# Optimization experiments

Measured on AMD Instinct MI355X. Metric: run time of the kernel, lower is better.

Reference implementation:

```python
import jax, jax.numpy as jnp
import numpy as np

H = 1024; NH = 16; L = 4; K = 128; N = 65536
ADIM_MOVE = 9; ADIM_TURN = 4; S = 2 * K + 2


def setup_inputs() -> dict:
    key = jax.random.key(0)
    ks = jax.random.split(key, 24)
    s = 0.02
    d = {}
    d['x'] = jax.random.normal(ks[0], (1, H), jnp.float32)
    d['memory_vectors'] = jax.random.normal(ks[1], (N, H), jnp.float32)
    d['memory_next_vectors'] = jax.random.normal(ks[2], (N, H), jnp.float32)
    d['memory_surprises'] = jax.random.uniform(ks[3], (N,), jnp.float32)
    d['memory_rewards'] = jax.random.normal(ks[4], (N,), jnp.float32)
    d['rand_noise'] = jax.random.uniform(ks[5], (N,), jnp.float32)
    d['action_idx_move'] = jax.random.randint(ks[6], (N,), 0, ADIM_MOVE)
    d['action_idx_turn'] = jax.random.randint(ks[7], (N,), 0, ADIM_TURN)
    d['start_token'] = jax.random.uniform(ks[8], (1, H)) * 2 - 1
    d['pos_emb'] = jax.random.uniform(ks[9], (S, H)) * 2 - 1
    d['in_proj_w'] = jax.random.normal(ks[10], (L, 3 * H, H)) * s
    d['in_proj_b'] = jnp.zeros((L, 3 * H))
    d['out_w'] = jax.random.normal(ks[11], (L, H, H)) * s
    d['out_b'] = jnp.zeros((L, H))
    d['ln1_w'] = jnp.ones((L, H)); d['ln1_b'] = jnp.zeros((L, H))
    d['ln2_w'] = jnp.ones((L, H)); d['ln2_b'] = jnp.zeros((L, H))
    d['ffn_w1'] = jax.random.normal(ks[12], (L, 4 * H, H)) * s
    d['ffn_b1'] = jnp.zeros((L, 4 * H))
    d['ffn_w2'] = jax.random.normal(ks[13], (L, H, 4 * H)) * s
    d['ffn_b2'] = jnp.zeros((L, H))
    d['act_move_w1'] = jax.random.normal(ks[14], (H, ADIM_MOVE)) * s
    d['act_move_b1'] = jnp.zeros((H,))
    d['act_move_w2'] = jax.random.normal(ks[15], (H, H)) * s
    d['act_move_b2'] = jnp.zeros((H,))
    d['act_turn_w1'] = jax.random.normal(ks[16], (H, ADIM_TURN)) * s
    d['act_turn_b1'] = jnp.zeros((H,))
    d['act_turn_w2'] = jax.random.normal(ks[17], (H, H)) * s
    d['act_turn_b2'] = jnp.zeros((H,))
    d['vh_w1'] = jax.random.normal(ks[18], (4 * H, H)) * s
    d['vh_b1'] = jnp.zeros((4 * H,))
    d['vh_w2'] = jax.random.normal(ks[19], (1, 4 * H)) * s
    d['vh_b2'] = jnp.zeros((1,))
    return d


def _get_scores(v):
    # tie-aware average rank / N (matches torch unique_consecutive logic)
    srt = jnp.sort(v)
    left = jnp.searchsorted(srt, v, side='left')
    right = jnp.searchsorted(srt, v, side='right')
    return ((left + right - 1).astype(v.dtype) / 2) / v.shape[0]


def _ln(x, w, b):
    m = x.mean(-1, keepdims=True)
    var = ((x - m) ** 2).mean(-1, keepdims=True)
    return (x - m) / jnp.sqrt(var + 1e-5) * w + b


def _gelu(x):
    return jax.nn.gelu(x, approximate=False)


def _mha(x, wqkv, bqkv, wo, bo, mask):
    dh = H // NH
    qkv = x @ wqkv.T + bqkv                      # [S, 3H]
    q, k, v = jnp.split(qkv, 3, axis=-1)
    q = q.reshape(-1, NH, dh); k = k.reshape(-1, NH, dh); v = v.reshape(-1, NH, dh)
    att = jnp.einsum('qhd,khd->hqk', q, k) / np.sqrt(dh).astype(np.float32)
    att = jax.nn.softmax(att + mask, axis=-1)
    o = jnp.einsum('hqk,khd->qhd', att, v).reshape(-1, H)
    return o @ wo.T + bo


def reference(x, memory_vectors, memory_next_vectors, memory_surprises, memory_rewards, rand_noise, action_idx_move, action_idx_turn, start_token, pos_emb, in_proj_w, in_proj_b, out_w, out_b, ln1_w, ln1_b, ln2_w, ln2_b, ffn_w1, ffn_b1, ffn_w2, ffn_b2, act_move_w1, act_move_b1, act_move_w2, act_move_b2, act_turn_w1, act_turn_b1, act_turn_w2, act_turn_b2, vh_w1, vh_b1, vh_w2, vh_b2):
    eps = 1e-8
    # ---- scoring (no_grad in original) ----
    xs = jax.lax.stop_gradient(x)
    xn = xs / jnp.maximum(jnp.linalg.norm(xs, axis=-1, keepdims=True), eps)
    mn = memory_vectors / jnp.maximum(jnp.linalg.norm(memory_vectors, axis=-1, keepdims=True), eps)
    sim = mn @ xn[0]                              # [N]
    scores = _get_scores(memory_surprises) ** 2 + _get_scores(sim) ** 2 + _get_scores(rand_noise) ** 2
    _, idx = jax.lax.top_k(scores, K)             # [K]
    # ---- gather memories + action one-hots ----
    sel = jax.lax.stop_gradient(memory_vectors[idx])   # [K, H]
    oh_move = jax.nn.one_hot(action_idx_move[idx], ADIM_MOVE, dtype=x.dtype)
    oh_turn = jax.nn.one_hot(action_idx_turn[idx], ADIM_TURN, dtype=x.dtype)
    av_move = _gelu(oh_move @ act_move_w1.T + act_move_b1) @ act_move_w2.T + act_move_b2
    av_turn = _gelu(oh_turn @ act_turn_w1.T + act_turn_b1) @ act_turn_w2.T + act_turn_b2
    av = (av_move + av_turn) / 2                  # mean over actions
    # interleave [v0, a0, v1, a1, ...], prepend start, append target
    vecs = jnp.stack((sel, av), axis=1).reshape(-1, H)
    vecs = jnp.concatenate((start_token, vecs, x), axis=0)   # [S, H]
    vecs = vecs + pos_emb
    mask = jnp.where(jnp.tril(jnp.ones((S, S), bool)), 0.0, -jnp.inf).astype(x.dtype)
    for l in range(L):
        vecs = vecs + _mha(_ln(vecs, ln1_w[l], ln1_b[l]), in_proj_w[l], in_proj_b[l], out_w[l], out_b[l], mask)
        h = _ln(vecs, ln2_w[l], ln2_b[l])
        vecs = vecs + _gelu(h @ ffn_w1[l].T + ffn_b1[l]) @ ffn_w2[l].T + ffn_b2[l]
    vidx = jnp.arange(K + 1) * 2 + 1
    vh_in = vecs[vidx]
    vp = _gelu(vh_in @ vh_w1.T + vh_b1) @ vh_w2.T + vh_b2   # [K+1, 1]
    sel_rewards = memory_rewards[idx]
    losses = (vp[:-1].ravel() - sel_rewards) ** 2            # mse, reduction='none'
    return (vecs[1:], memory_next_vectors[idx], vp[-1], losses, sel_rewards)
```

## Files before the change

kernel.cpp:

```cpp
#include <hip/hip_runtime.h>
#include <hip/hip_bf16.h>
#include <math.h>
#include <stdint.h>

typedef unsigned int u32;
typedef unsigned long long u64;

#define NM   65536
#define HD   1024
#define KS   128
#define SQ   258
#define NL   4
#define NBIN 65536
#define CCAP 2048

using bf16x8 = __attribute__((ext_vector_type(8))) short;
using f32x4v = __attribute__((ext_vector_type(4))) float;

struct Ctrl { u32 b1, above1, T, candcnt; };

static constexpr size_t A256(size_t x){ return (x + 255) & ~(size_t)255; }

constexpr size_t OFF_H3   = 0;
constexpr size_t OFF_C3   = OFF_H3 + (size_t)3*NBIN*4;
constexpr size_t OFF_HS   = OFF_C3 + (size_t)3*NBIN*4;
constexpr size_t ZERO_BYTES = OFF_HS + (size_t)NBIN*4;
constexpr size_t OFF_BS   = A256(ZERO_BYTES);
constexpr size_t OFF_BB   = A256(OFF_BS + 192*4);
constexpr size_t OFF_VPB  = A256(OFF_BB + 192*4);
constexpr size_t OFF_XN   = A256(OFF_VPB + 1024);
constexpr size_t OFF_P3   = A256(OFF_XN + (size_t)HD*4);
constexpr size_t OFF_K3   = A256(OFF_P3 + (size_t)3*(NBIN+1)*4);
constexpr size_t OFF_L3   = A256(OFF_K3 + (size_t)3*NM*4);
constexpr size_t OFF_KSC  = A256(OFF_L3 + (size_t)3*NM*4);
constexpr size_t OFF_CAND = A256(OFF_KSC + (size_t)NM*4);
constexpr size_t OFF_CTRL = A256(OFF_CAND + (size_t)CCAP*8);
constexpr size_t OFF_IDX  = A256(OFF_CTRL + 256);
constexpr size_t OFF_HM   = A256(OFF_IDX  + (size_t)KS*4);
constexpr size_t OFF_HT   = A256(OFF_HM   + (size_t)KS*HD*4);
constexpr size_t OFF_REW  = A256(OFF_HT   + (size_t)KS*HD*4);
constexpr size_t OFF_VECS = A256(OFF_REW  + (size_t)KS*4);
constexpr size_t OFF_LNB  = A256(OFF_VECS + (size_t)SQ*HD*4);
constexpr size_t OFF_QKV  = A256(OFF_LNB  + (size_t)SQ*HD*4);
constexpr size_t OFF_ATT  = A256(OFF_QKV  + (size_t)SQ*3*HD*4);
constexpr size_t OFF_FFH  = A256(OFF_ATT  + (size_t)SQ*HD*4);
constexpr size_t OFF_PART = A256(OFF_FFH  + (size_t)SQ*4*HD*4);

constexpr int OUT_NEXT = 257*HD;
constexpr int OUT_VP   = OUT_NEXT + KS*HD;
constexpr int OUT_LOSS = OUT_VP + 1;
constexpr int OUT_REWO = OUT_LOSS + KS;

__device__ __forceinline__ float gelu_f(float v){
  return 0.5f*v*(1.0f + erff(v*0.70710678118654752440f));
}

__device__ __forceinline__ short f2bf(float f){
  __hip_bfloat16 h = __float2bfloat16(f);
  short s;
  __builtin_memcpy(&s, &h, sizeof(short));
  return s;
}

__device__ __forceinline__ u32 fkey(float v){
  u32 b = __float_as_uint(v);
  return (b >> 31) ? ~b : (b | 0x80000000u);
}

__global__ void k_xn(const float* __restrict__ x, float* __restrict__ xn){
  __shared__ float red[256];
  int t = threadIdx.x;
  float s = 0.f;
  for(int i=t;i<HD;i+=256){ float v=x[i]; s += v*v; }
  red[t]=s; __syncthreads();
  for(int o=128;o>0;o>>=1){ if(t<o) red[t]+=red[t+o]; __syncthreads(); }
  float nrm = fmaxf(sqrtf(red[0]), 1e-8f);
  for(int i=t;i<HD;i+=256) xn[i] = x[i]/nrm;
}

__global__ __launch_bounds__(256) void k_simkey(const float* __restrict__ mv, const float* __restrict__ xn,
                                                const float* __restrict__ surp, const float* __restrict__ noise,
                                                u32* __restrict__ keys3, u32* __restrict__ hist3){
  __shared__ float xs[HD];
  int t = threadIdx.x;
  for(int i=t;i<HD;i+=256) xs[i]=xn[i];
  __syncthreads();
  int lane = t & 63, w = t >> 6;
  int row = blockIdx.x*4 + w;
  const float4* p = (const float4*)(mv + (size_t)row*HD);
  const float4* q = (const float4*)xs;
  float d=0.f, ss=0.f;
  #pragma unroll
  for(int r=0;r<4;++r){
    float4 v = p[lane + 64*r]; float4 u = q[lane + 64*r];
    d  += v.x*u.x + v.y*u.y + v.z*u.z + v.w*u.w;
    ss += v.x*v.x + v.y*v.y + v.z*v.z + v.w*v.w;
  }
  for(int off=32;off>0;off>>=1){ d += __shfl_xor(d,off,64); ss += __shfl_xor(ss,off,64); }
  if(lane==0){
    float sim = d / fmaxf(sqrtf(ss),1e-8f);
    float vals[3] = { surp[row], sim, noise[row] };
    #pragma unroll
    for(int a=0;a<3;++a){
      u32 k = fkey(vals[a]);
      keys3[(size_t)a*NM + row] = k;
      atomicAdd(&hist3[(size_t)a*NBIN + (k >> 16)], 1u);
    }
  }
}

__global__ __launch_bounds__(256) void k_scanA(const u32* __restrict__ hist3, u32* __restrict__ bsum){
  __shared__ u32 red[256];
  int blk = blockIdx.x;
  int t = threadIdx.x;
  const u32* h = hist3 + (size_t)(blk>>6)*NBIN + (size_t)(blk&63)*1024;
  u32 s = 0;
  #pragma unroll
  for(int j=0;j<4;++j) s += h[t*4+j];
  red[t]=s; __syncthreads();
  for(int o=128;o>0;o>>=1){ if(t<o) red[t]+=red[t+o]; __syncthreads(); }
  if(t==0) bsum[blk] = red[0];
}

__global__ __launch_bounds__(256) void k_scanB(const u32* __restrict__ bsum, u32* __restrict__ bbase,
                                               u32* __restrict__ pref3){
  __shared__ u32 incl[256];
  int t = threadIdx.x;
  u32 v = (t < 192) ? bsum[t] : 0u;
  incl[t] = v; __syncthreads();
  for(int off=1;off<256;off<<=1){
    u32 u = (t >= off) ? incl[t-off] : 0u;
    __syncthreads(); incl[t] += u; __syncthreads();
  }
  if(t < 192){
    int a = t >> 6;
    u32 excl_t = incl[t] - v;
    u32 excl_a = incl[a*64] - bsum[a*64];
    bbase[t] = excl_t - excl_a;
  }
  if(t < 3) pref3[(size_t)t*(NBIN+1) + NBIN] = NM;
}

__global__ __launch_bounds__(256) void k_scanC(const u32* __restrict__ hist3, const u32* __restrict__ bbase,
                                               u32* __restrict__ pref3){
  __shared__ u32 part[256];
  int blk = blockIdx.x;
  int t = threadIdx.x;
  int a = blk >> 6, c = blk & 63;
  const u32* h = hist3 + (size_t)a*NBIN + (size_t)c*1024;
  u32* pref = pref3 + (size_t)a*(NBIN+1) + (size_t)c*1024;
  u32 loc[4]; u32 s = 0;
  #pragma unroll
  for(int j=0;j<4;++j){ loc[j] = h[t*4+j]; s += loc[j]; }
  part[t] = s; __syncthreads();
  for(int off=1;off<256;off<<=1){
    u32 u = (t >= off) ? part[t-off] : 0u;
    __syncthreads(); part[t] += u; __syncthreads();
  }
  u32 run = bbase[blk] + part[t] - s;
  #pragma unroll
  for(int j=0;j<4;++j){ pref[t*4+j] = run; run += loc[j]; }
}

__global__ void k_scatter3(const u32* __restrict__ keys3, const u32* __restrict__ pref3,
                           u32* __restrict__ cnt3, u32* __restrict__ lo3){
  int i = blockIdx.x*256 + threadIdx.x;
  if(i >= NM) return;
  #pragma unroll
  for(int a=0;a<3;++a){
    u32 k = keys3[(size_t)a*NM + i];
    u32 b = k >> 16;
    u32 pos = pref3[(size_t)a*(NBIN+1) + b] + atomicAdd(&cnt3[(size_t)a*NBIN + b], 1u);
    lo3[(size_t)a*NM + pos] = k & 0xFFFFu;
  }
}

__global__ void k_rank3score(const u32* __restrict__ keys3, const u32* __restrict__ pref3,
                             const u32* __restrict__ lo3, u32* __restrict__ keysS, u32* __restrict__ histS){
  int i = blockIdx.x*256 + threadIdx.x;
  if(i >= NM) return;
  float rr[3];
  #pragma unroll
  for(int a=0;a<3;++a){
    u32 k = keys3[(size_t)a*NM + i];
    u32 b = k >> 16, my = k & 0xFFFFu;
    const u32* pref = pref3 + (size_t)a*(NBIN+1);
    const u32* lo = lo3 + (size_t)a*NM;
    u32 s = pref[b], e = pref[b+1];
    u32 nl = 0, ne = 0;
    for(u32 j=s;j<e;++j){ u32 u = lo[j]; nl += (u < my); ne += (u == my); }
    u32 left = s + nl, right = left + ne;
    rr[a] = (float)(left + right - 1) * (1.0f/131072.0f);
  }
  float sc = __fadd_rn(__fadd_rn(__fmul_rn(rr[0],rr[0]), __fmul_rn(rr[1],rr[1])), __fmul_rn(rr[2],rr[2]));
  u32 k = __float_as_uint(sc);
  keysS[i] = k;
  atomicAdd(&histS[k >> 16], 1u);
}

__global__ __launch_bounds__(1024) void k_sel1(const u32* __restrict__ hist, Ctrl* ctrl){
  __shared__ u32 part[1024];
  int t = threadIdx.x;
  u32 base = t*64, s = 0;
  for(int j=0;j<64;++j) s += hist[base+j];
  part[t] = s; __syncthreads();
  for(int off=1;off<1024;off<<=1){
    u32 v = (t+off < 1024) ? part[t+off] : 0u;
    __syncthreads(); part[t] += v; __syncthreads();
  }
  u32 above = part[t] - s;
  if(above < (u32)KS && above + s >= (u32)KS){
    u32 cum = above;
    for(int j=63;j>=0;--j){
      u32 c = hist[base+j];
      if(cum + c >= (u32)KS){ ctrl->T = (u32)(base+j) << 16; ctrl->candcnt = 0; break; }
      cum += c;
    }
  }
}

__global__ void k_collect(const u32* __restrict__ keys, Ctrl* ctrl, u64* __restrict__ cand){
  int i = blockIdx.x*256 + threadIdx.x;
  if(i >= NM) return;
  u32 k = keys[i];
  if(k >= ctrl->T){
    u32 p = atomicAdd(&ctrl->candcnt, 1u);
    if(p < (u32)CCAP) cand[p] = ((u64)(~k) << 32) | (u32)i;
  }
}

__global__ __launch_bounds__(1024) void k_sortsel(const u64* __restrict__ cand, const Ctrl* ctrl, int* __restrict__ idx){
  __shared__ u64 sm[CCAP];
  int t = threadIdx.x;
  u32 n = ctrl->candcnt; if(n > (u32)CCAP) n = CCAP;
  for(int i=t;i<CCAP;i+=1024) sm[i] = (i < (int)n) ? cand[i] : 0xFFFFFFFFFFFFFFFFull;
  __syncthreads();
  for(int k=2;k<=CCAP;k<<=1){
    for(int j=k>>1;j>0;j>>=1){
      for(int i=t;i<CCAP;i+=1024){
        int ixj = i ^ j;
        if(ixj > i){
          bool up = ((i & k) == 0);
          u64 a = sm[i], b = sm[ixj];
          if((a > b) == up){ sm[i] = b; sm[ixj] = a; }
        }
      }
      __syncthreads();
    }
  }
  if(t < KS) idx[t] = (int)(sm[t] & 0xFFFFFFFFu);
}

__global__ void k_gather(const int* __restrict__ idx,
                         const float* __restrict__ mv, const float* __restrict__ mnv,
                         const float* __restrict__ mrew,
                         const int* __restrict__ aim, const int* __restrict__ ait,
                         const float* __restrict__ amw1, const float* __restrict__ amb1,
                         const float* __restrict__ atw1, const float* __restrict__ atb1,
                         const float* __restrict__ start, const float* __restrict__ x,
                         const float* __restrict__ pos,
                         float* __restrict__ vecs, float* __restrict__ outnext,
                         float* __restrict__ hm, float* __restrict__ ht,
                         float* __restrict__ rew, float* __restrict__ outrew){
  int k = blockIdx.x;
  int t = threadIdx.x;
  if(k < KS){
    int row = idx[k];
    const float* a = mv  + (size_t)row*HD;
    const float* b = mnv + (size_t)row*HD;
    const float* pz = pos + (size_t)(2*k+1)*HD;
    float* vr = vecs + (size_t)(2*k+1)*HD;
    for(int c=t;c<HD;c+=256){
      vr[c] = a[c] + pz[c];
      outnext[(size_t)k*HD+c] = b[c];
    }
    int am = aim[row], at = ait[row];
    for(int j=t;j<HD;j+=256){
      hm[(size_t)k*HD+j] = gelu_f(amw1[(size_t)j*9 + am] + amb1[j]);
      ht[(size_t)k*HD+j] = gelu_f(atw1[(size_t)j*4 + at] + atb1[j]);
    }
    if(t == 0){ float r = mrew[row]; rew[k] = r; outrew[k] = r; }
  } else {
    for(int c=t;c<HD;c+=256){
      vecs[c] = start[c] + pos[c];
      vecs[(size_t)(SQ-1)*HD + c] = x[c] + pos[(size_t)(SQ-1)*HD + c];
    }
  }
}

__device__ __forceinline__ void gemm_body(char* smem, const float* __restrict__ A, const float* __restrict__ B,
        float* __restrict__ P, int M, int N, int K, int S, int nbm, int lda, int tile){
  short* As = (short*)smem;
  short* Bs = (short*)(smem + 8192);
  int bm = (tile % nbm) * 64;
  int tmp = tile / nbm;
  int z  = tmp % S;
  int bn = (tmp / S) * 64;
  int Ks = K / S, kbeg = z*Ks;
  int nk = Ks >> 5;

  int t = threadIdx.x;
  int srow = t >> 2, sg = t & 3;
  int sgp = sg ^ ((srow >> 1) & 3);
  bool arow_ok = (bm + srow) < M;
  const float* ap = A + (size_t)(bm + srow)*lda + kbeg + sg*8;
  const float* bp = B + (size_t)(bn + srow)*K + kbeg + sg*8;
  int stoff = srow*32 + sgp*8;

  int lane = t & 63, w = t >> 6;
  int wm = (w >> 1)*32, wn = (w & 1)*32;
  int lr = lane & 15, lg = lane >> 4;
  int ra0 = wm + lr, ra1 = ra0 + 16;
  int rb0 = wn + lr, rb1 = rb0 + 16;
  int aoff0 = ra0*32 + (lg ^ ((ra0>>1)&3))*8;
  int aoff1 = ra1*32 + (lg ^ ((ra1>>1)&3))*8;
  int boff0 = rb0*32 + (lg ^ ((rb0>>1)&3))*8;
  int boff1 = rb1*32 + (lg ^ ((rb1>>1)&3))*8;

  f32x4v acc00 = {0,0,0,0}, acc01 = {0,0,0,0}, acc10 = {0,0,0,0}, acc11 = {0,0,0,0};

  {
    float4 va0 = {0,0,0,0}, va1 = {0,0,0,0};
    if(arow_ok){ va0 = *(const float4*)ap; va1 = *(const float4*)(ap+4); }
    float4 vb0 = *(const float4*)bp;
    float4 vb1 = *(const float4*)(bp+4);
    ap += 32; bp += 32;
    bf16x8 sa, sb;
    sa[0]=f2bf(va0.x); sa[1]=f2bf(va0.y); sa[2]=f2bf(va0.z); sa[3]=f2bf(va0.w);
    sa[4]=f2bf(va1.x); sa[5]=f2bf(va1.y); sa[6]=f2bf(va1.z); sa[7]=f2bf(va1.w);
    sb[0]=f2bf(vb0.x); sb[1]=f2bf(vb0.y); sb[2]=f2bf(vb0.z); sb[3]=f2bf(vb0.w);
    sb[4]=f2bf(vb1.x); sb[5]=f2bf(vb1.y); sb[6]=f2bf(vb1.z); sb[7]=f2bf(vb1.w);
    *(bf16x8*)&As[stoff] = sa;
    *(bf16x8*)&Bs[stoff] = sb;
  }
  __syncthreads();

  for(int kk = 0; kk < nk; ++kk){
    int cur = (kk & 1) << 11;
    bool more = (kk + 1) < nk;
    float4 va0, va1, vb0, vb1;
    if(more){
      va0 = make_float4(0,0,0,0); va1 = make_float4(0,0,0,0);
      if(arow_ok){ va0 = *(const float4*)ap; va1 = *(const float4*)(ap+4); }
      vb0 = *(const float4*)bp;
      vb1 = *(const float4*)(bp+4);
      ap += 32; bp += 32;
    }
    bf16x8 a0 = *(const bf16x8*)&As[cur + aoff0];
    bf16x8 a1 = *(const bf16x8*)&As[cur + aoff1];
    bf16x8 b0 = *(const bf16x8*)&Bs[cur + boff0];
    bf16x8 b1 = *(const bf16x8*)&Bs[cur + boff1];
    acc00 = __builtin_amdgcn_mfma_f32_16x16x32_bf16(a0, b0, acc00, 0, 0, 0);
    acc01 = __builtin_amdgcn_mfma_f32_16x16x32_bf16(a0, b1, acc01, 0, 0, 0);
    acc10 = __builtin_amdgcn_mfma_f32_16x16x32_bf16(a1, b0, acc10, 0, 0, 0);
    acc11 = __builtin_amdgcn_mfma_f32_16x16x32_bf16(a1, b1, acc11, 0, 0, 0);
    if(more){
      int nxt = cur ^ 2048;
      bf16x8 sa, sb;
      sa[0]=f2bf(va0.x); sa[1]=f2bf(va0.y); sa[2]=f2bf(va0.z); sa[3]=f2bf(va0.w);
      sa[4]=f2bf(va1.x); sa[5]=f2bf(va1.y); sa[6]=f2bf(va1.z); sa[7]=f2bf(va1.w);
      sb[0]=f2bf(vb0.x); sb[1]=f2bf(vb0.y); sb[2]=f2bf(vb0.z); sb[3]=f2bf(vb0.w);
      sb[4]=f2bf(vb1.x); sb[5]=f2bf(vb1.y); sb[6]=f2bf(vb1.z); sb[7]=f2bf(vb1.w);
      *(bf16x8*)&As[nxt + stoff] = sa;
      *(bf16x8*)&Bs[nxt + stoff] = sb;
    }
    __syncthreads();
  }

  size_t zbase = (size_t)z * (size_t)M;
  #pragma unroll
  for(int r=0;r<4;++r){
    int row0 = bm + wm + lg*4 + r;
    int row1 = row0 + 16;
    int c0 = bn + wn + lr, c1 = c0 + 16;
    if(row0 < M){
      P[(zbase+row0)*N + c0] = acc00[r];
      P[(zbase+row0)*N + c1] = acc01[r];
    }
    if(row1 < M){
      P[(zbase+row1)*N + c0] = acc10[r];
      P[(zbase+row1)*N + c1] = acc11[r];
    }
  }
}

__global__ __launch_bounds__(256) void k_gemm(const float* __restrict__ A, const float* __restrict__ B,
        float* __restrict__ P, int M, int N, int K, int S, int nbm, int lda){
  __shared__ char smem[16384];
  u32 nwg = gridDim.x, orig = blockIdx.x;
  u32 swz = (orig & 7)*(nwg >> 3) + (orig >> 3);
  gemm_body(smem, A, B, P, M, N, K, S, nbm, lda, (int)swz);
}

__global__ __launch_bounds__(256) void k_actgemm(const float* __restrict__ hm, const float* __restrict__ ht,
        const float* __restrict__ amw2, const float* __restrict__ atw2,
        float* __restrict__ part, float* __restrict__ part2){
  __shared__ char smem[16384];
  int which = blockIdx.x >> 8, tile = blockIdx.x & 255;
  gemm_body(smem, which ? ht : hm, which ? atw2 : amw2, which ? part2 : part,
            KS, HD, HD, 8, 2, HD, tile);
}

template<int S_, int ACT>
__global__ __launch_bounds__(256) void k_finS(const float* __restrict__ P, const float* __restrict__ bias,
                                              float* __restrict__ C, int MN4, int Nd){
  int i4 = blockIdx.x*256 + threadIdx.x;
  if(i4 >= MN4) return;
  size_t off = (size_t)i4*4;
  size_t MN = (size_t)MN4*4;
  float4 v = *(const float4*)&P[off];
  #pragma unroll
  for(int z=1;z<S_;++z){
    float4 q = *(const float4*)&P[(size_t)z*MN + off];
    v.x += q.x; v.y += q.y; v.z += q.z; v.w += q.w;
  }
  int j = (i4 % (Nd/4))*4;
  float4 b4 = *(const float4*)&bias[j];
  v.x += b4.x; v.y += b4.y; v.z += b4.z; v.w += b4.w;
  if(ACT == 1){ v.x = gelu_f(v.x); v.y = gelu_f(v.y); v.z = gelu_f(v.z); v.w = gelu_f(v.w); }
  *(float4*)&C[off] = v;
}

template<int S_, bool LN>
__global__ __launch_bounds__(256) void k_finrow(const float* __restrict__ P, const float* __restrict__ bias,
                                                float* __restrict__ vecs, const float* __restrict__ lw,
                                                const float* __restrict__ lb, float* __restrict__ dst){
  __shared__ float red[256];
  int row = blockIdx.x, t = threadIdx.x;
  int j = t*4;
  float4 v = *(const float4*)&P[(size_t)row*HD + j];
  #pragma unroll
  for(int z=1;z<S_;++z){
    float4 p = *(const float4*)&P[((size_t)z*SQ + row)*HD + j];
    v.x += p.x; v.y += p.y; v.z += p.z; v.w += p.w;
  }
  float4 b4 = *(const float4*)&bias[j];
  float4 r4 = *(const float4*)&vecs[(size_t)row*HD + j];
  v.x += b4.x + r4.x; v.y += b4.y + r4.y; v.z += b4.z + r4.z; v.w += b4.w + r4.w;
  *(float4*)&vecs[(size_t)row*HD + j] = v;
  if(LN){
    red[t] = v.x+v.y+v.z+v.w; __syncthreads();
    for(int o=128;o>0;o>>=1){ if(t<o) red[t]+=red[t+o]; __syncthreads(); }
    float m = red[0]*(1.0f/HD); __syncthreads();
    float dx=v.x-m, dy=v.y-m, dz=v.z-m, dw=v.w-m;
    red[t] = dx*dx+dy*dy+dz*dz+dw*dw; __syncthreads();
    for(int o=128;o>0;o>>=1){ if(t<o) red[t]+=red[t+o]; __syncthreads(); }
    float den = sqrtf(red[0]*(1.0f/HD) + 1e-5f);
    float4 w4 = *(const float4*)&lw[j];
    float4 lb4 = *(const float4*)&lb[j];
    float4 o4;
    o4.x = dx/den*w4.x + lb4.x; o4.y = dy/den*w4.y + lb4.y;
    o4.z = dz/den*w4.z + lb4.z; o4.w = dw/den*w4.w + lb4.w;
    *(float4*)&dst[(size_t)row*HD + j] = o4;
  } else {
    if(row >= 1) *(float4*)&dst[(size_t)(row-1)*HD + j] = v;
  }
}

__global__ __launch_bounds__(256) void k_finavln(const float* __restrict__ Pm, const float* __restrict__ Pt,
                                                 const float* __restrict__ bm_, const float* __restrict__ bt_,
                                                 const float* __restrict__ pos, float* __restrict__ vecs,
                                                 const float* __restrict__ lw, const float* __restrict__ lb,
                                                 float* __restrict__ lnb){
  __shared__ float red[256];
  int row = blockIdx.x, t = threadIdx.x;
  int j = t*4;
  float4 v;
  if(row >= 2 && row <= 256 && ((row & 1) == 0)){
    int k = (row-2) >> 1;
    float4 s = {0,0,0,0};
    #pragma unroll
    for(int z=0;z<8;++z){
      float4 a = *(const float4*)&Pm[((size_t)z*KS + k)*HD + j];
      float4 b = *(const float4*)&Pt[((size_t)z*KS + k)*HD + j];
      s.x += a.x+b.x; s.y += a.y+b.y; s.z += a.z+b.z; s.w += a.w+b.w;
    }
    float4 bm4 = *(const float4*)&bm_[j];
    float4 bt4 = *(const float4*)&bt_[j];
    float4 p4 = *(const float4*)&pos[(size_t)row*HD + j];
    v.x = 0.5f*(s.x + bm4.x + bt4.x) + p4.x;
    v.y = 0.5f*(s.y + bm4.y + bt4.y) + p4.y;
    v.z = 0.5f*(s.z + bm4.z + bt4.z) + p4.z;
    v.w = 0.5f*(s.w + bm4.w + bt4.w) + p4.w;
    *(float4*)&vecs[(size_t)row*HD + j] = v;
  } else {
    v = *(const float4*)&vecs[(size_t)row*HD + j];
  }
  red[t] = v.x+v.y+v.z+v.w; __syncthreads();
  for(int o=128;o>0;o>>=1){ if(t<o) red[t]+=red[t+o]; __syncthreads(); }
  float m = red[0]*(1.0f/HD); __syncthreads();
  float dx=v.x-m, dy=v.y-m, dz=v.z-m, dw=v.w-m;
  red[t] = dx*dx+dy*dy+dz*dz+dw*dw; __syncthreads();
  for(int o=128;o>0;o>>=1){ if(t<o) red[t]+=red[t+o]; __syncthreads(); }
  float den = sqrtf(red[0]*(1.0f/HD) + 1e-5f);
  float4 w4 = *(const float4*)&lw[j];
  float4 lb4 = *(const float4*)&lb[j];
  float4 o4;
  o4.x = dx/den*w4.x + lb4.x; o4.y = dy/den*w4.y + lb4.y;
  o4.z = dz/den*w4.z + lb4.z; o4.w = dw/den*w4.w + lb4.w;
  *(float4*)&lnb[(size_t)row*HD + j] = o4;
}

__global__ void k_attn(const float* __restrict__ qkv, float* __restrict__ outp){
  __shared__ float qv[64];
  __shared__ float p[SQ];
  __shared__ float red[256];
  int q = blockIdx.x, h = blockIdx.y, t = threadIdx.x;
  if(t < 64) qv[t] = qkv[(size_t)q*3072 + h*64 + t];
  __syncthreads();
  int nk = q + 1;
  float lmax = -1e30f;
  for(int j=t;j<nk;j+=256){
    const float* kr = qkv + (size_t)j*3072 + 1024 + h*64;
    float d = 0.f;
    for(int c=0;c<64;++c) d += qv[c]*kr[c];
    d *= 0.125f;
    p[j] = d;
    lmax = fmaxf(lmax, d);
  }
  red[t] = lmax; __syncthreads();
  for(int o=128;o>0;o>>=1){ if(t<o) red[t] = fmaxf(red[t], red[t+o]); __syncthreads(); }
  float m = red[0];
  __syncthreads();
  float lsum = 0.f;
  for(int j=t;j<nk;j+=256){ float e = expf(p[j]-m); p[j] = e; lsum += e; }
  red[t] = lsum; __syncthreads();
  for(int o=128;o>0;o>>=1){ if(t<o) red[t] += red[t+o]; __syncthreads(); }
  float inv = 1.0f/red[0];
  __syncthreads();
  int d = t & 63, g = t >> 6;
  float acc = 0.f;
  for(int j=g;j<nk;j+=4) acc += p[j]*qkv[(size_t)j*3072 + 2048 + h*64 + d];
  red[t] = acc; __syncthreads();
  if(g == 0){
    float o4 = red[d] + red[64+d] + red[128+d] + red[192+d];
    outp[(size_t)q*HD + h*64 + d] = o4*inv;
  }
}

__global__ __launch_bounds__(256) void k_vpfin(const float* __restrict__ P, const float* __restrict__ vb1,
                                               const float* __restrict__ vw2, float* __restrict__ vp){
  __shared__ float red[256];
  int r = blockIdx.x, t = threadIdx.x;
  float s = 0.f;
  for(int c=t;c<4096;c+=256){
    float v = P[(size_t)r*4096 + c];
    #pragma unroll
    for(int z=1;z<4;++z) v += P[((size_t)z*129 + r)*4096 + c];
    s += gelu_f(v + vb1[c]) * vw2[c];
  }
  red[t]=s; __syncthreads();
  for(int o=128;o>0;o>>=1){ if(t<o) red[t]+=red[t+o]; __syncthreads(); }
  if(t == 0) vp[r] = red[0];
}

__global__ void k_outsmall(const float* __restrict__ vp, const float* __restrict__ b2,
                           const float* __restrict__ rew, float* __restrict__ outp){
  int t = threadIdx.x;
  float bb = b2[0];
  if(t == 0) outp[OUT_VP] = vp[KS] + bb;
  if(t < KS){
    float d = (vp[t] + bb) - rew[t];
    outp[OUT_LOSS + t] = d*d;
    outp[OUT_REWO + t] = rew[t];
  }
}

extern "C" void kernel_launch(void* const* d_in, const int* in_sizes, int n_in,
                              void* d_out, int out_size, void* d_ws, size_t ws_size,
                              hipStream_t stream){
  const float* x     = (const float*)d_in[0];
  const float* mv    = (const float*)d_in[1];
  const float* mnv   = (const float*)d_in[2];
  const float* surp  = (const float*)d_in[3];
  const float* mrew  = (const float*)d_in[4];
  const float* noise = (const float*)d_in[5];
  const int*   aim   = (const int*)d_in[6];
  const int*   ait   = (const int*)d_in[7];
  const float* start = (const float*)d_in[8];
  const float* pos   = (const float*)d_in[9];
  const float* inW = (const float*)d_in[10]; const float* inB = (const float*)d_in[11];
  const float* oW  = (const float*)d_in[12]; const float* oB  = (const float*)d_in[13];
  const float* l1w = (const float*)d_in[14]; const float* l1b = (const float*)d_in[15];
  const float* l2w = (const float*)d_in[16]; const float* l2b = (const float*)d_in[17];
  const float* f1w = (const float*)d_in[18]; const float* f1b = (const float*)d_in[19];
  const float* f2w = (const float*)d_in[20]; const float* f2b = (const float*)d_in[21];
  const float* amw1= (const float*)d_in[22]; const float* amb1= (const float*)d_in[23];
  const float* amw2= (const float*)d_in[24]; const float* amb2= (const float*)d_in[25];
  const float* atw1= (const float*)d_in[26]; const float* atb1= (const float*)d_in[27];
  const float* atw2= (const float*)d_in[28]; const float* atb2= (const float*)d_in[29];
  const float* vw1 = (const float*)d_in[30]; const float* vb1 = (const float*)d_in[31];
  const float* vw2 = (const float*)d_in[32]; const float* vb2 = (const float*)d_in[33];

  float* out = (float*)d_out;
  char* ws = (char*)d_ws;
  u32*  hist3 = (u32*)(ws+OFF_H3);
  u32*  cnt3  = (u32*)(ws+OFF_C3);
  u32*  histS = (u32*)(ws+OFF_HS);
  u32*  bsum  = (u32*)(ws+OFF_BS);
  u32*  bbase = (u32*)(ws+OFF_BB);
  float* vp   = (float*)(ws+OFF_VPB);
  float* xn   = (float*)(ws+OFF_XN);
  u32*  pref3 = (u32*)(ws+OFF_P3);
  u32*  keys3 = (u32*)(ws+OFF_K3);
  u32*  lo3   = (u32*)(ws+OFF_L3);
  u32*  keysS = (u32*)(ws+OFF_KSC);
  u64*  cand  = (u64*)(ws+OFF_CAND);
  Ctrl* ctrl  = (Ctrl*)(ws+OFF_CTRL);
  int*  idxb  = (int*)(ws+OFF_IDX);
  float* hm   = (float*)(ws+OFF_HM);
  float* ht   = (float*)(ws+OFF_HT);
  float* rew  = (float*)(ws+OFF_REW);
  float* vecs = (float*)(ws+OFF_VECS);
  float* lnb  = (float*)(ws+OFF_LNB);
  float* qkvb = (float*)(ws+OFF_QKV);
  float* attn = (float*)(ws+OFF_ATT);
  float* ffh  = (float*)(ws+OFF_FFH);
  float* part = (float*)(ws+OFF_PART);
  float* part2= part + (size_t)8*KS*HD;

  dim3 b256(256);
  int gN = NM/256;

  (void)hipMemsetAsync(ws, 0, ZERO_BYTES, stream);

  hipLaunchKernelGGL(k_xn, dim3(1), b256, 0, stream, x, xn);
  hipLaunchKernelGGL(k_simkey, dim3(NM/4), b256, 0, stream, mv, xn, surp, noise, keys3, hist3);
  hipLaunchKernelGGL(k_scanA, dim3(192), b256, 0, stream, hist3, bsum);
  hipLaunchKernelGGL(k_scanB, dim3(1), b256, 0, stream, bsum, bbase, pref3);
  hipLaunchKernelGGL(k_scanC, dim3(192), b256, 0, stream, hist3, bbase, pref3);
  hipLaunchKernelGGL(k_scatter3, dim3(gN), b256, 0, stream, keys3, pref3, cnt3, lo3);
  hipLaunchKernelGGL(k_rank3score, dim3(gN), b256, 0, stream, keys3, pref3, lo3, keysS, histS);
  hipLaunchKernelGGL(k_sel1, dim3(1), dim3(1024), 0, stream, histS, ctrl);
  hipLaunchKernelGGL(k_collect, dim3(gN), b256, 0, stream, keysS, ctrl, cand);
  hipLaunchKernelGGL(k_sortsel, dim3(1), dim3(1024), 0, stream, cand, ctrl, idxb);

  hipLaunchKernelGGL(k_gather, dim3(KS+1), b256, 0, stream, idxb, mv, mnv, mrew, aim, ait,
                     amw1, amb1, atw1, atb1, start, x, pos,
                     vecs, out + OUT_NEXT, hm, ht, rew, out + OUT_REWO);
  hipLaunchKernelGGL(k_actgemm, dim3(512), b256, 0, stream, hm, ht, amw2, atw2, part, part2);
  hipLaunchKernelGGL(k_finavln, dim3(SQ), b256, 0, stream, part, part2, amb2, atb2, pos, vecs, l1w, l1b, lnb);

  for(int l=0;l<NL;++l){
    hipLaunchKernelGGL(k_gemm, dim3(480), b256, 0, stream, lnb, inW + (size_t)l*3*HD*HD, part, SQ, 3*HD, HD, 2, 5, HD);
    hipLaunchKernelGGL((k_finS<2,0>), dim3(774), b256, 0, stream, part, inB + (size_t)l*3*HD, qkvb, SQ*3*HD/4, 3*HD);
    hipLaunchKernelGGL(k_attn, dim3(SQ, 16), b256, 0, stream, qkvb, attn);
    hipLaunchKernelGGL(k_gemm, dim3(640), b256, 0, stream, attn, oW + (size_t)l*HD*HD, part, SQ, HD, HD, 8, 5, HD);
    hipLaunchKernelGGL((k_finrow<8,true>), dim3(SQ), b256, 0, stream, part, oB + (size_t)l*HD, vecs,
                       l2w + (size_t)l*HD, l2b + (size_t)l*HD, lnb);
    hipLaunchKernelGGL(k_gemm, dim3(640), b256, 0, stream, lnb, f1w + (size_t)l*4*HD*HD, part, SQ, 4*HD, HD, 2, 5, HD);
    hipLaunchKernelGGL((k_finS<2,1>), dim3(1032), b256, 0, stream, part, f1b + (size_t)l*4*HD, ffh, SQ*4*HD/4, 4*HD);
    hipLaunchKernelGGL(k_gemm, dim3(640), b256, 0, stream, ffh, f2w + (size_t)l*HD*4*HD, part, SQ, HD, 4*HD, 8, 5, 4*HD);
    if(l < NL-1)
      hipLaunchKernelGGL((k_finrow<8,true>), dim3(SQ), b256, 0, stream, part, f2b + (size_t)l*HD, vecs,
                         l1w + (size_t)(l+1)*HD, l1b + (size_t)(l+1)*HD, lnb);
    else
      hipLaunchKernelGGL((k_finrow<8,false>), dim3(SQ), b256, 0, stream, part, f2b + (size_t)l*HD, vecs,
                         (const float*)nullptr, (const float*)nullptr, out);
  }

  hipLaunchKernelGGL(k_gemm, dim3(768), b256, 0, stream, vecs + HD, vw1, part, KS+1, 4*HD, HD, 4, 3, 2*HD);
  hipLaunchKernelGGL(k_vpfin, dim3(KS+1), b256, 0, stream, part, vb1, vw2, vp);
  hipLaunchKernelGGL(k_outsmall, dim3(1), b256, 0, stream, vp, vb2, rew, out);
}
```

Baseline: 972.7 us.

## Pre-convert weights to bf16 and stream GEMM tiles into LDS directly

Adds a kernel that converts all transformer, action and value-head weight matrices to bf16 in a workspace on every call. Intermediate activations (LN outputs, attention output, FFN hidden, value-head input) are now written as bf16. The GEMM body loads its tiles with global_load_lds (direct global-to-LDS, 16 bytes per lane) instead of fp32 loads followed by in-register conversion. This removes the per-tile convert work and halves the bytes the GEMMs read, at the cost of an extra full pass over roughly 57M weight elements each call. The GEMMs also drop the row bound check on A, so tail tiles read past the valid rows into adjacent workspace.

```diff
diff --git a/kernel.cpp b/kernel.cpp
--- a/kernel.cpp
+++ b/kernel.cpp
@@ -4,6 +4,7 @@
 #include <stdint.h>
 
 typedef unsigned int u32;
+typedef unsigned short u16;
 typedef unsigned long long u64;
 
 #define NM   65536
@@ -36,15 +37,26 @@
 constexpr size_t OFF_CAND = A256(OFF_KSC + (size_t)NM*4);
 constexpr size_t OFF_CTRL = A256(OFF_CAND + (size_t)CCAP*8);
 constexpr size_t OFF_IDX  = A256(OFF_CTRL + 256);
-constexpr size_t OFF_HM   = A256(OFF_IDX  + (size_t)KS*4);
-constexpr size_t OFF_HT   = A256(OFF_HM   + (size_t)KS*HD*4);
-constexpr size_t OFF_REW  = A256(OFF_HT   + (size_t)KS*HD*4);
-constexpr size_t OFF_VECS = A256(OFF_REW  + (size_t)KS*4);
+constexpr size_t OFF_REW  = A256(OFF_IDX  + (size_t)KS*4);
+constexpr size_t OFF_HM   = A256(OFF_REW  + (size_t)KS*4);
+constexpr size_t OFF_HT   = A256(OFF_HM   + (size_t)KS*HD*2);
+constexpr size_t OFF_VECS = A256(OFF_HT   + (size_t)KS*HD*2);
 constexpr size_t OFF_LNB  = A256(OFF_VECS + (size_t)SQ*HD*4);
-constexpr size_t OFF_QKV  = A256(OFF_LNB  + (size_t)SQ*HD*4);
+constexpr size_t OFF_QKV  = A256(OFF_LNB  + (size_t)SQ*HD*2);
 constexpr size_t OFF_ATT  = A256(OFF_QKV  + (size_t)SQ*3*HD*4);
-constexpr size_t OFF_FFH  = A256(OFF_ATT  + (size_t)SQ*HD*4);
-constexpr size_t OFF_PART = A256(OFF_FFH  + (size_t)SQ*4*HD*4);
+constexpr size_t OFF_FFH  = A256(OFF_ATT  + (size_t)SQ*HD*2);
+constexpr size_t OFF_VHIN = A256(OFF_FFH  + (size_t)SQ*4*HD*2);
+constexpr size_t OFF_WB   = A256(OFF_VHIN + (size_t)129*HD*2);
+constexpr size_t NWELEM   = 56623104;
+constexpr size_t OFF_PART = A256(OFF_WB + NWELEM*2);
+
+constexpr size_t WB_IN = 0;
+constexpr size_t WB_O  = WB_IN + (size_t)4*3*HD*HD;
+constexpr size_t WB_F1 = WB_O  + (size_t)4*HD*HD;
+constexpr size_t WB_F2 = WB_F1 + (size_t)4*4*HD*HD;
+constexpr size_t WB_AM = WB_F2 + (size_t)4*4*HD*HD;
+constexpr size_t WB_AT = WB_AM + (size_t)HD*HD;
+constexpr size_t WB_VH = WB_AT + (size_t)HD*HD;
 
 constexpr int OUT_NEXT = 257*HD;
 constexpr int OUT_VP   = OUT_NEXT + KS*HD;
@@ -55,16 +67,40 @@
   return 0.5f*v*(1.0f + erff(v*0.70710678118654752440f));
 }
 
-__device__ __forceinline__ short f2bf(float f){
+__device__ __forceinline__ u16 f2bf(float f){
   __hip_bfloat16 h = __float2bfloat16(f);
-  short s;
-  __builtin_memcpy(&s, &h, sizeof(short));
+  u16 s;
+  __builtin_memcpy(&s, &h, sizeof(u16));
   return s;
 }
 
 __device__ __forceinline__ u32 fkey(float v){
   u32 b = __float_as_uint(v);
   return (b >> 31) ? ~b : (b | 0x80000000u);
+}
+
+__device__ __forceinline__ void gload16(const u16* g, u16* l){
+  __builtin_amdgcn_global_load_lds(
+      (const __attribute__((address_space(1))) unsigned int*)g,
+      (__attribute__((address_space(3))) unsigned int*)l, 16, 0, 0);
+}
+
+struct WSeg { const float* s; u16* d; u32 base4, end4; };
+struct WCA { WSeg seg[7]; u32 tot4; };
+__global__ __launch_bounds__(256) void k_wconv(WCA a){
+  u32 i = blockIdx.x*256 + threadIdx.x;
+  if(i >= a.tot4) return;
+  #pragma unroll
+  for(int j=0;j<7;++j){
+    if(i < a.seg[j].end4){
+      u32 off = i - a.seg[j].base4;
+      float4 v = *(const float4*)&a.seg[j].s[(size_t)off*4];
+      u16 r[4] = { f2bf(v.x), f2bf(v.y), f2bf(v.z), f2bf(v.w) };
+      u64 pk; __builtin_memcpy(&pk, r, 8);
+      *(u64*)&a.seg[j].d[(size_t)off*4] = pk;
+      return;
+    }
+  }
 }
 
 __global__ void k_xn(const float* __restrict__ x, float* __restrict__ xn){
@@ -260,7 +296,7 @@
                          const float* __restrict__ start, const float* __restrict__ x,
                          const float* __restrict__ pos,
                          float* __restrict__ vecs, float* __restrict__ outnext,
-                         float* __restrict__ hm, float* __restrict__ ht,
+                         u16* __restrict__ hm, u16* __restrict__ ht,
                          float* __restrict__ rew, float* __restrict__ outrew){
   int k = blockIdx.x;
   int t = threadIdx.x;
@@ -276,8 +312,8 @@
     }
     int am = aim[row], at = ait[row];
     for(int j=t;j<HD;j+=256){
-      hm[(size_t)k*HD+j] = gelu_f(amw1[(size_t)j*9 + am] + amb1[j]);
-      ht[(size_t)k*HD+j] = gelu_f(atw1[(size_t)j*4 + at] + atb1[j]);
+      hm[(size_t)k*HD+j] = f2bf(gelu_f(amw1[(size_t)j*9 + am] + amb1[j]));
+      ht[(size_t)k*HD+j] = f2bf(gelu_f(atw1[(size_t)j*4 + at] + atb1[j]));
     }
     if(t == 0){ float r = mrew[row]; rew[k] = r; outrew[k] = r; }
   } else {
@@ -288,10 +324,8 @@
   }
 }
 
-__device__ __forceinline__ void gemm_body(char* smem, const float* __restrict__ A, const float* __restrict__ B,
+__device__ __forceinline__ void gemm_body(u16* As, u16* Bs, const u16* __restrict__ A, const u16* __restrict__ B,
         float* __restrict__ P, int M, int N, int K, int S, int nbm, int lda, int tile){
-  short* As = (short*)smem;
-  short* Bs = (short*)(smem + 8192);
   int bm = (tile % nbm) * 64;
   int tmp = tile / nbm;
   int z  = tmp % S;
@@ -299,52 +333,37 @@
   int Ks = K / S, kbeg = z*Ks;
   int nk = Ks >> 5;
 
-  int t = threadIdx.x;
-  int srow = t >> 2, sg = t & 3;
-  int sgp = sg ^ ((srow >> 1) & 3);
-  bool arow_ok = (bm + srow) < M;
-  const float* ap = A + (size_t)(bm + srow)*lda + kbeg + sg*8;
-  const float* bp = B + (size_t)(bn + srow)*K + kbeg + sg*8;
-  int stoff = srow*32 + sgp*8;
-
-  int lane = t & 63, w = t >> 6;
+  int t = threadIdx.x, lane = t & 63, w = t >> 6;
+  int srow = w*16 + (lane >> 2);
+  int clog = (lane & 3) ^ ((srow >> 1) & 3);
+  const u16* ga = A + (size_t)(bm + srow)*lda + kbeg + clog*8;
+  const u16* gb = B + (size_t)(bn + srow)*K  + kbeg + clog*8;
+  u16* la = As + w*512;
+  u16* lb = Bs + w*512;
+
   int wm = (w >> 1)*32, wn = (w & 1)*32;
   int lr = lane & 15, lg = lane >> 4;
-  int ra0 = wm + lr, ra1 = ra0 + 16;
-  int rb0 = wn + lr, rb1 = rb0 + 16;
-  int aoff0 = ra0*32 + (lg ^ ((ra0>>1)&3))*8;
-  int aoff1 = ra1*32 + (lg ^ ((ra1>>1)&3))*8;
-  int boff0 = rb0*32 + (lg ^ ((rb0>>1)&3))*8;
-  int boff1 = rb1*32 + (lg ^ ((rb1>>1)&3))*8;
+  int r0 = wm + lr, r1 = r0 + 16;
+  int c0 = wn + lr, c1 = c0 + 16;
+  int aoff0 = r0*32 + ((lg ^ ((r0>>1)&3))*8);
+  int aoff1 = r1*32 + ((lg ^ ((r1>>1)&3))*8);
+  int boff0 = c0*32 + ((lg ^ ((c0>>1)&3))*8);
+  int boff1 = c1*32 + ((lg ^ ((c1>>1)&3))*8);
 
   f32x4v acc00 = {0,0,0,0}, acc01 = {0,0,0,0}, acc10 = {0,0,0,0}, acc11 = {0,0,0,0};
 
-  {
-    float4 va0 = {0,0,0,0}, va1 = {0,0,0,0};
-    if(arow_ok){ va0 = *(const float4*)ap; va1 = *(const float4*)(ap+4); }
-    float4 vb0 = *(const float4*)bp;
-    float4 vb1 = *(const float4*)(bp+4);
-    ap += 32; bp += 32;
-    bf16x8 sa, sb;
-    sa[0]=f2bf(va0.x); sa[1]=f2bf(va0.y); sa[2]=f2bf(va0.z); sa[3]=f2bf(va0.w);
-    sa[4]=f2bf(va1.x); sa[5]=f2bf(va1.y); sa[6]=f2bf(va1.z); sa[7]=f2bf(va1.w);
-    sb[0]=f2bf(vb0.x); sb[1]=f2bf(vb0.y); sb[2]=f2bf(vb0.z); sb[3]=f2bf(vb0.w);
-    sb[4]=f2bf(vb1.x); sb[5]=f2bf(vb1.y); sb[6]=f2bf(vb1.z); sb[7]=f2bf(vb1.w);
-    *(bf16x8*)&As[stoff] = sa;
-    *(bf16x8*)&Bs[stoff] = sb;
-  }
+  gload16(ga, la);
+  gload16(gb, lb);
+  ga += 32; gb += 32;
   __syncthreads();
 
   for(int kk = 0; kk < nk; ++kk){
-    int cur = (kk & 1) << 11;
-    bool more = (kk + 1) < nk;
-    float4 va0, va1, vb0, vb1;
-    if(more){
-      va0 = make_float4(0,0,0,0); va1 = make_float4(0,0,0,0);
-      if(arow_ok){ va0 = *(const float4*)ap; va1 = *(const float4*)(ap+4); }
-      vb0 = *(const float4*)bp;
-      vb1 = *(const float4*)(bp+4);
-      ap += 32; bp += 32;
+    int cur = (kk & 1) * 2048;
+    if(kk + 1 < nk){
+      int nxt = 2048 - cur;
+      gload16(ga, la + nxt);
+      gload16(gb, lb + nxt);
+      ga += 32; gb += 32;
     }
     bf16x8 a0 = *(const bf16x8*)&As[cur + aoff0];
     bf16x8 a1 = *(const bf16x8*)&As[cur + aoff1];
@@ -354,16 +373,6 @@
     acc01 = __builtin_amdgcn_mfma_f32_16x16x32_bf16(a0, b1, acc01, 0, 0, 0);
     acc10 = __builtin_amdgcn_mfma_f32_16x16x32_bf16(a1, b0, acc10, 0, 0, 0);
     acc11 = __builtin_amdgcn_mfma_f32_16x16x32_bf16(a1, b1, acc11, 0, 0, 0);
-    if(more){
-      int nxt = cur ^ 2048;
-      bf16x8 sa, sb;
-      sa[0]=f2bf(va0.x); sa[1]=f2bf(va0.y); sa[2]=f2bf(va0.z); sa[3]=f2bf(va0.w);
-      sa[4]=f2bf(va1.x); sa[5]=f2bf(va1.y); sa[6]=f2bf(va1.z); sa[7]=f2bf(va1.w);
-      sb[0]=f2bf(vb0.x); sb[1]=f2bf(vb0.y); sb[2]=f2bf(vb0.z); sb[3]=f2bf(vb0.w);
-      sb[4]=f2bf(vb1.x); sb[5]=f2bf(vb1.y); sb[6]=f2bf(vb1.z); sb[7]=f2bf(vb1.w);
-      *(bf16x8*)&As[nxt + stoff] = sa;
-      *(bf16x8*)&Bs[nxt + stoff] = sb;
-    }
     __syncthreads();
   }
 
@@ -372,38 +381,40 @@
   for(int r=0;r<4;++r){
     int row0 = bm + wm + lg*4 + r;
     int row1 = row0 + 16;
-    int c0 = bn + wn + lr, c1 = c0 + 16;
+    int cc0 = bn + wn + lr, cc1 = cc0 + 16;
     if(row0 < M){
-      P[(zbase+row0)*N + c0] = acc00[r];
-      P[(zbase+row0)*N + c1] = acc01[r];
+      P[(zbase+row0)*N + cc0] = acc00[r];
+      P[(zbase+row0)*N + cc1] = acc01[r];
     }
     if(row1 < M){
-      P[(zbase+row1)*N + c0] = acc10[r];
-      P[(zbase+row1)*N + c1] = acc11[r];
-    }
-  }
-}
-
-__global__ __launch_bounds__(256) void k_gemm(const float* __restrict__ A, const float* __restrict__ B,
+      P[(zbase+row1)*N + cc0] = acc10[r];
+      P[(zbase+row1)*N + cc1] = acc11[r];
+    }
+  }
+}
+
+__global__ __launch_bounds__(256) void k_gemm(const u16* __restrict__ A, const u16* __restrict__ B,
         float* __restrict__ P, int M, int N, int K, int S, int nbm, int lda){
-  __shared__ char smem[16384];
+  __shared__ u16 As[4096];
+  __shared__ u16 Bs[4096];
   u32 nwg = gridDim.x, orig = blockIdx.x;
   u32 swz = (orig & 7)*(nwg >> 3) + (orig >> 3);
-  gemm_body(smem, A, B, P, M, N, K, S, nbm, lda, (int)swz);
-}
-
-__global__ __launch_bounds__(256) void k_actgemm(const float* __restrict__ hm, const float* __restrict__ ht,
-        const float* __restrict__ amw2, const float* __restrict__ atw2,
+  gemm_body(As, Bs, A, B, P, M, N, K, S, nbm, lda, (int)swz);
+}
+
+__global__ __launch_bounds__(256) void k_actgemm(const u16* __restrict__ hm, const u16* __restrict__ ht,
+        const u16* __restrict__ amw2, const u16* __restrict__ atw2,
         float* __restrict__ part, float* __restrict__ part2){
-  __shared__ char smem[16384];
+  __shared__ u16 As[4096];
+  __shared__ u16 Bs[4096];
   int which = blockIdx.x >> 8, tile = blockIdx.x & 255;
-  gemm_body(smem, which ? ht : hm, which ? atw2 : amw2, which ? part2 : part,
+  gemm_body(As, Bs, which ? ht : hm, which ? atw2 : amw2, which ? part2 : part,
             KS, HD, HD, 8, 2, HD, tile);
 }
 
-template<int S_, int ACT>
+template<int S_, int ACT, bool BF>
 __global__ __launch_bounds__(256) void k_finS(const float* __restrict__ P, const float* __restrict__ bias,
-                                              float* __restrict__ C, int MN4, int Nd){
+                                              float* __restrict__ C, u16* __restrict__ Cb, int MN4, int Nd){
   int i4 = blockIdx.x*256 + threadIdx.x;
   if(i4 >= MN4) return;
   size_t off = (size_t)i4*4;
@@ -418,13 +429,20 @@
   float4 b4 = *(const float4*)&bias[j];
   v.x += b4.x; v.y += b4.y; v.z += b4.z; v.w += b4.w;
   if(ACT == 1){ v.x = gelu_f(v.x); v.y = gelu_f(v.y); v.z = gelu_f(v.z); v.w = gelu_f(v.w); }
-  *(float4*)&C[off] = v;
+  if(BF){
+    u16 r[4] = { f2bf(v.x), f2bf(v.y), f2bf(v.z), f2bf(v.w) };
+    u64 pk; __builtin_memcpy(&pk, r, 8);
+    *(u64*)&Cb[off] = pk;
+  } else {
+    *(float4*)&C[off] = v;
+  }
 }
 
 template<int S_, bool LN>
 __global__ __launch_bounds__(256) void k_finrow(const float* __restrict__ P, const float* __restrict__ bias,
                                                 float* __restrict__ vecs, const float* __restrict__ lw,
-                                                const float* __restrict__ lb, float* __restrict__ dst){
+                                                const float* __restrict__ lb, u16* __restrict__ lnb,
+                                                float* __restrict__ outp, u16* __restrict__ vhin){
   __shared__ float red[256];
   int row = blockIdx.x, t = threadIdx.x;
   int j = t*4;
@@ -448,12 +466,18 @@
     float den = sqrtf(red[0]*(1.0f/HD) + 1e-5f);
     float4 w4 = *(const float4*)&lw[j];
     float4 lb4 = *(const float4*)&lb[j];
-    float4 o4;
-    o4.x = dx/den*w4.x + lb4.x; o4.y = dy/den*w4.y + lb4.y;
-    o4.z = dz/den*w4.z + lb4.z; o4.w = dw/den*w4.w + lb4.w;
-    *(float4*)&dst[(size_t)row*HD + j] = o4;
+    u16 r[4] = { f2bf(dx/den*w4.x + lb4.x), f2bf(dy/den*w4.y + lb4.y),
+                 f2bf(dz/den*w4.z + lb4.z), f2bf(dw/den*w4.w + lb4.w) };
+    u64 pk; __builtin_memcpy(&pk, r, 8);
+    *(u64*)&lnb[(size_t)row*HD + j] = pk;
   } else {
-    if(row >= 1) *(float4*)&dst[(size_t)(row-1)*HD + j] = v;
+    if(row >= 1) *(float4*)&outp[(size_t)(row-1)*HD + j] = v;
+    if(row & 1){
+      int vr = (row-1) >> 1;
+      u16 r[4] = { f2bf(v.x), f2bf(v.y), f2bf(v.z), f2bf(v.w) };
+      u64 pk; __builtin_memcpy(&pk, r, 8);
+      *(u64*)&vhin[(size_t)vr*HD + j] = pk;
+    }
   }
 }
 
@@ -461,7 +485,7 @@
                                                  const float* __restrict__ bm_, const float* __restrict__ bt_,
                                                  const float* __restrict__ pos, float* __restrict__ vecs,
                                                  const float* __restrict__ lw, const float* __restrict__ lb,
-                                                 float* __restrict__ lnb){
+                                                 u16* __restrict__ lnb){
   __shared__ float red[256];
   int row = blockIdx.x, t = threadIdx.x;
   int j = t*4;
@@ -495,13 +519,13 @@
   float den = sqrtf(red[0]*(1.0f/HD) + 1e-5f);
   float4 w4 = *(const float4*)&lw[j];
   float4 lb4 = *(const float4*)&lb[j];
-  float4 o4;
-  o4.x = dx/den*w4.x + lb4.x; o4.y = dy/den*w4.y + lb4.y;
-  o4.z = dz/den*w4.z + lb4.z; o4.w = dw/den*w4.w + lb4.w;
-  *(float4*)&lnb[(size_t)row*HD + j] = o4;
-}
-
-__global__ void k_attn(const float* __restrict__ qkv, float* __restrict__ outp){
+  u16 r[4] = { f2bf(dx/den*w4.x + lb4.x), f2bf(dy/den*w4.y + lb4.y),
+               f2bf(dz/den*w4.z + lb4.z), f2bf(dw/den*w4.w + lb4.w) };
+  u64 pk; __builtin_memcpy(&pk, r, 8);
+  *(u64*)&lnb[(size_t)row*HD + j] = pk;
+}
+
+__global__ void k_attn(const float* __restrict__ qkv, u16* __restrict__ outp){
   __shared__ float qv[64];
   __shared__ float p[SQ];
   __shared__ float red[256];
@@ -534,7 +558,7 @@
   red[t] = acc; __syncthreads();
   if(g == 0){
     float o4 = red[d] + red[64+d] + red[128+d] + red[192+d];
-    outp[(size_t)q*HD + h*64 + d] = o4*inv;
+    outp[(size_t)q*HD + h*64 + d] = f2bf(o4*inv);
   }
 }
 
@@ -608,21 +632,45 @@
   u64*  cand  = (u64*)(ws+OFF_CAND);
   Ctrl* ctrl  = (Ctrl*)(ws+OFF_CTRL);
   int*  idxb  = (int*)(ws+OFF_IDX);
-  float* hm   = (float*)(ws+OFF_HM);
-  float* ht   = (float*)(ws+OFF_HT);
   float* rew  = (float*)(ws+OFF_REW);
+  u16*  hm    = (u16*)(ws+OFF_HM);
+  u16*  ht    = (u16*)(ws+OFF_HT);
   float* vecs = (float*)(ws+OFF_VECS);
-  float* lnb  = (float*)(ws+OFF_LNB);
+  u16*  lnb   = (u16*)(ws+OFF_LNB);
   float* qkvb = (float*)(ws+OFF_QKV);
-  float* attn = (float*)(ws+OFF_ATT);
-  float* ffh  = (float*)(ws+OFF_FFH);
+  u16*  attn  = (u16*)(ws+OFF_ATT);
+  u16*  ffh   = (u16*)(ws+OFF_FFH);
+  u16*  vhin  = (u16*)(ws+OFF_VHIN);
+  u16*  wb    = (u16*)(ws+OFF_WB);
   float* part = (float*)(ws+OFF_PART);
   float* part2= part + (size_t)8*KS*HD;
 
+  u16* inW_bf = wb + WB_IN;
+  u16* oW_bf  = wb + WB_O;
+  u16* f1w_bf = wb + WB_F1;
+  u16* f2w_bf = wb + WB_F2;
+  u16* am_bf  = wb + WB_AM;
+  u16* at_bf  = wb + WB_AT;
+  u16* vh_bf  = wb + WB_VH;
+
   dim3 b256(256);
   int gN = NM/256;
 
   (void)hipMemsetAsync(ws, 0, ZERO_BYTES, stream);
+
+  {
+    WCA a;
+    const float* srcs[7] = { inW, oW, f1w, f2w, amw2, atw2, vw1 };
+    u16* dsts[7] = { inW_bf, oW_bf, f1w_bf, f2w_bf, am_bf, at_bf, vh_bf };
+    u32 sizes4[7] = { 4*3*HD*HD/4, 4*HD*HD/4, 4*4*HD*HD/4, 4*4*HD*HD/4, HD*HD/4, HD*HD/4, 4*HD*HD/4 };
+    u32 cum = 0;
+    for(int j=0;j<7;++j){
+      a.seg[j].s = srcs[j]; a.seg[j].d = dsts[j];
+      a.seg[j].base4 = cum; cum += sizes4[j]; a.seg[j].end4 = cum;
+    }
+    a.tot4 = cum;
+    hipLaunchKernelGGL(k_wconv, dim3((cum + 255)/256), b256, 0, stream, a);
+  }
 
   hipLaunchKernelGGL(k_xn, dim3(1), b256, 0, stream, x, xn);
   hipLaunchKernelGGL(k_simkey, dim3(NM/4), b256, 0, stream, mv, xn, surp, noise, keys3, hist3);
@@ -638,28 +686,28 @@
   hipLaunchKernelGGL(k_gather, dim3(KS+1), b256, 0, stream, idxb, mv, mnv, mrew, aim, ait,
                      amw1, amb1, atw1, atb1, start, x, pos,
                      vecs, out + OUT_NEXT, hm, ht, rew, out + OUT_REWO);
-  hipLaunchKernelGGL(k_actgemm, dim3(512), b256, 0, stream, hm, ht, amw2, atw2, part, part2);
+  hipLaunchKernelGGL(k_actgemm, dim3(512), b256, 0, stream, hm, ht, am_bf, at_bf, part, part2);
   hipLaunchKernelGGL(k_finavln, dim3(SQ), b256, 0, stream, part, part2, amb2, atb2, pos, vecs, l1w, l1b, lnb);
 
   for(int l=0;l<NL;++l){
-    hipLaunchKernelGGL(k_gemm, dim3(480), b256, 0, stream, lnb, inW + (size_t)l*3*HD*HD, part, SQ, 3*HD, HD, 2, 5, HD);
-    hipLaunchKernelGGL((k_finS<2,0>), dim3(774), b256, 0, stream, part, inB + (size_t)l*3*HD, qkvb, SQ*3*HD/4, 3*HD);
+    hipLaunchKernelGGL(k_gemm, dim3(480), b256, 0, stream, lnb, inW_bf + (size_t)l*3*HD*HD, part, SQ, 3*HD, HD, 2, 5, HD);
+    hipLaunchKernelGGL((k_finS<2,0,false>), dim3(774), b256, 0, stream, part, inB + (size_t)l*3*HD, qkvb, (u16*)nullptr, SQ*3*HD/4, 3*HD);
     hipLaunchKernelGGL(k_attn, dim3(SQ, 16), b256, 0, stream, qkvb, attn);
-    hipLaunchKernelGGL(k_gemm, dim3(640), b256, 0, stream, attn, oW + (size_t)l*HD*HD, part, SQ, HD, HD, 8, 5, HD);
+    hipLaunchKernelGGL(k_gemm, dim3(640), b256, 0, stream, attn, oW_bf + (size_t)l*HD*HD, part, SQ, HD, HD, 8, 5, HD);
     hipLaunchKernelGGL((k_finrow<8,true>), dim3(SQ), b256, 0, stream, part, oB + (size_t)l*HD, vecs,
-                       l2w + (size_t)l*HD, l2b + (size_t)l*HD, lnb);
-    hipLaunchKernelGGL(k_gemm, dim3(640), b256, 0, stream, lnb, f1w + (size_t)l*4*HD*HD, part, SQ, 4*HD, HD, 2, 5, HD);
-    hipLaunchKernelGGL((k_finS<2,1>), dim3(1032), b256, 0, stream, part, f1b + (size_t)l*4*HD, ffh, SQ*4*HD/4, 4*HD);
-    hipLaunchKernelGGL(k_gemm, dim3(640), b256, 0, stream, ffh, f2w + (size_t)l*HD*4*HD, part, SQ, HD, 4*HD, 8, 5, 4*HD);
+                       l2w + (size_t)l*HD, l2b + (size_t)l*HD, lnb, (float*)nullptr, (u16*)nullptr);
+    hipLaunchKernelGGL(k_gemm, dim3(640), b256, 0, stream, lnb, f1w_bf + (size_t)l*4*HD*HD, part, SQ, 4*HD, HD, 2, 5, HD);
+    hipLaunchKernelGGL((k_finS<2,1,true>), dim3(1032), b256, 0, stream, part, f1b + (size_t)l*4*HD, (float*)nullptr, ffh, SQ*4*HD/4, 4*HD);
+    hipLaunchKernelGGL(k_gemm, dim3(640), b256, 0, stream, ffh, f2w_bf + (size_t)l*HD*4*HD, part, SQ, HD, 4*HD, 8, 5, 4*HD);
     if(l < NL-1)
       hipLaunchKernelGGL((k_finrow<8,true>), dim3(SQ), b256, 0, stream, part, f2b + (size_t)l*HD, vecs,
-                         l1w + (size_t)(l+1)*HD, l1b + (size_t)(l+1)*HD, lnb);
+                         l1w + (size_t)(l+1)*HD, l1b + (size_t)(l+1)*HD, lnb, (float*)nullptr, (u16*)nullptr);
     else
       hipLaunchKernelGGL((k_finrow<8,false>), dim3(SQ), b256, 0, stream, part, f2b + (size_t)l*HD, vecs,
-                         (const float*)nullptr, (const float*)nullptr, out);
-  }
-
-  hipLaunchKernelGGL(k_gemm, dim3(768), b256, 0, stream, vecs + HD, vw1, part, KS+1, 4*HD, HD, 4, 3, 2*HD);
+                         (const float*)nullptr, (const float*)nullptr, (u16*)nullptr, out, vhin);
+  }
+
+  hipLaunchKernelGGL(k_gemm, dim3(768), b256, 0, stream, vhin, vh_bf, part, KS+1, 4*HD, HD, 4, 3, HD);
   hipLaunchKernelGGL(k_vpfin, dim3(KS+1), b256, 0, stream, part, vb1, vw2, vp);
   hipLaunchKernelGGL(k_outsmall, dim3(1), b256, 0, stream, vp, vb2, rew, out);
 }
```

After: 947.5 us. 2.6% less time.
